# Performance work log

Hardware: AMD Instinct MI355X
Metric: run time of the kernel (lower is better)

The kernel has to match this reference:

```python
import jax, jax.numpy as jnp
import numpy as np


def _rot_mat(thetas, scales):
    # thetas, scales: [bs, g] -> [bs, g, 9, 9] bilinear-interpolation matrices
    bs, g = thetas.shape
    t = thetas.reshape(-1)
    s = scales.reshape(-1)
    x = jnp.cos(t) * s
    y = jnp.sin(t) * s
    yp = -y
    z = jnp.zeros_like(x)
    o = jnp.ones_like(x)
    a = x - y; b = x * y; c = x + y; d = a * c; e = a + c
    ap = x - yp; bp = x * yp; cp = x + yp; dp = ap * cp; ep = ap + cp

    def M(rows):
        # rows: 9 lists of 9 [N]-arrays -> [9, 9, N]
        return jnp.stack([jnp.stack(r, axis=0) for r in rows], axis=0)

    ctr = [z, z, z, z, o, z, z, z, z]

    pb1 = M([
        [a, 1 - a, z, z, z, z, z, z, z],
        [z, 1 - y, y, z, z, z, z, z, z],
        [z, z, a, z, z, 1 - a, z, z, z],
        [y, z, z, 1 - y, z, z, z, z, z],
        ctr,
        [z, z, z, z, z, 1 - y, z, z, y],
        [z, z, z, 1 - a, z, z, a, z, z],
        [z, z, z, z, z, z, y, 1 - y, z],
        [z, z, z, z, z, z, z, 1 - a, a]])
    pb2 = M([
        [a, 1 - a, z, z, z, z, z, z, z],
        [z, x - b, b, z, 1 - c + b, y - b, z, z, z],
        [z, z, a, z, z, 1 - a, z, z, z],
        [b, y - b, z, x - b, 1 - c + b, z, z, z, z],
        ctr,
        [z, z, z, z, 1 - c + b, x - b, z, y - b, b],
        [z, z, z, 1 - a, z, z, a, z, z],
        [z, z, z, y - b, 1 - c + b, z, b, x - b, z],
        [z, z, z, z, z, z, z, 1 - a, a]])
    ps1 = M([
        [d, a - d, z, c - d, 1 - e + d, z, z, z, z],
        [z, x - b, b, z, 1 - c + b, y - b, z, z, z],
        [z, c - d, d, z, 1 - e + d, a - d, z, z, z],
        [b, y - b, z, x - b, 1 - c + b, z, z, z, z],
        ctr,
        [z, z, z, z, 1 - c + b, x - b, z, y - b, b],
        [z, z, z, a - d, 1 - e + d, z, d, c - d, z],
        [z, z, z, y - b, 1 - c + b, z, b, x - b, z],
        [z, z, z, z, 1 - e + d, c - d, z, a - d, d]])
    ps2 = pb2  # identical in the source
    nb1 = M([
        [cp, z, z, 1 - cp, z, z, z, z, z],
        [yp, 1 - yp, z, z, z, z, z, z, z],
        [z, 1 - cp, cp, z, z, z, z, z, z],
        [z, z, z, 1 - yp, z, z, yp, z, z],
        ctr,
        [z, z, yp, z, z, 1 - yp, z, z, z],
        [z, z, z, z, z, z, cp, 1 - cp, z],
        [z, z, z, z, z, z, z, 1 - yp, yp],
        [z, z, z, z, z, 1 - cp, z, z, cp]])
    nb2 = M([
        [cp, z, z, 1 - cp, z, z, z, z, z],
        [bp, x - bp, z, yp - bp, 1 - cp + bp, z, z, z, z],
        [z, 1 - cp, cp, z, z, z, z, z, z],
        [z, z, z, x - bp, 1 - cp + bp, z, bp, yp - bp, z],
        ctr,
        [z, yp - bp, bp, z, 1 - cp + bp, x - bp, z, z, z],
        [z, z, z, z, z, z, cp, 1 - cp, z],
        [z, z, z, z, 1 - cp + bp, yp - bp, z, x - bp, bp],
        [z, z, z, z, z, 1 - cp, z, z, cp]])
    ns1 = M([
        [dp, cp - dp, z, ap - dp, 1 - ep + dp, z, z, z, z],
        [bp, x - bp, z, yp - bp, 1 - cp + bp, z, z, z, z],
        [z, ap - dp, dp, z, 1 - ep + dp, cp - dp, z, z, z],
        [z, yp - bp, bp, z, 1 - cp + bp, x - bp, z, z, z],
        ctr,
        [z, z, z, x - bp, 1 - cp + bp, z, bp, yp - bp, z],
        [z, z, z, cp - dp, 1 - ep + dp, z, dp, ap - dp, z],
        [z, z, z, z, 1 - cp + bp, yp - bp, z, x - bp, bp],
        [z, z, z, z, 1 - ep + dp, ap - dp, z, cp - dp, dp]])
    ns2 = nb2  # mirrors the positive branch where small_2 == big_2

    m_pos = (t >= 0.0)[None, None, :]
    m_big = (s >= 1.0)[None, None, :]
    m_1 = (jnp.abs(t) <= jnp.pi / 4)[None, None, :]
    pos = jnp.where(m_big, jnp.where(m_1, pb1, pb2), jnp.where(m_1, ps1, ps2))
    neg = jnp.where(m_big, jnp.where(m_1, nb1, nb2), jnp.where(m_1, ns1, ns2))
    rot = jnp.where(m_pos, pos, neg)  # [9, 9, bs*g]
    return jnp.transpose(rot, (2, 0, 1)).reshape(bs, g, 9, 9)


def _forward(x, thetas, scales, lambdas, weight):
    # x: [B, Cin, H, W]; weight: [n, Cout, Cin, 3, 3]; thetas/scales/lambdas: [B, n]
    B, Cin, H, W = x.shape
    n, Cout = weight.shape[0], weight.shape[1]
    rot = _rot_mat(thetas, scales) * lambdas[:, :, None, None]  # [B, n, 9, 9]
    w9 = weight.reshape(n, Cout, Cin, 9)
    # per-sample transformed kernel: sum over kernel_number n and source taps j
    w = jnp.einsum('bnij,nocj->bioc', rot, w9)  # [B, 9, Cout, Cin]
    w = jnp.transpose(w, (0, 2, 3, 1)).reshape(B * Cout, Cin, 3, 3)
    xg = x.reshape(1, B * Cin, H, W)
    out = jax.lax.conv_general_dilated(
        xg, w, window_strides=(1, 1), padding=((1, 1), (1, 1)),
        dimension_numbers=('NCHW', 'OIHW', 'NCHW'), feature_group_count=B)
    return out.reshape(B, Cout, H, W)


def setup_inputs() -> dict:
    key = jax.random.key(0)
    ks = jax.random.split(key, 5)
    B, Cin, Cout, H, W, n = 16, 256, 256, 64, 64, 4
    x = jax.random.normal(ks[0], (B, Cin, H, W), dtype=jnp.float32)
    thetas = jax.random.uniform(ks[1], (B, n), minval=-1.2, maxval=1.2, dtype=jnp.float32)
    scales = jax.random.uniform(ks[2], (B, n), minval=0.5, maxval=1.5, dtype=jnp.float32)
    lambdas = jax.nn.softmax(jax.random.normal(ks[3], (B, n), dtype=jnp.float32), axis=-1)
    weight = jax.random.normal(ks[4], (n, Cout, Cin, 3, 3), dtype=jnp.float32) * 0.05
    return {"x": x, "thetas": thetas, "scales": scales, "lambdas": lambdas, "weight": weight}


def reference(x, thetas, scales, lambdas, weight):
    return _forward(x, thetas, scales, lambdas, weight)
```

## Files before the change

### kernel.cpp

```cpp
#include <hip/hip_runtime.h>
#include <cstdint>
#include <cstddef>

typedef unsigned short ushort_t;
typedef __attribute__((ext_vector_type(4))) float f32x4;
typedef __attribute__((ext_vector_type(8))) short s16x8;

#define PI_4F 0.78539816339744830962f

__device__ inline ushort_t f2bf(float f) {
  unsigned int u = __float_as_uint(f);
  u = u + 0x7fffu + ((u >> 16) & 1u);
  return (ushort_t)(u >> 16);
}

__device__ void rot_compute(float t, float s, float* M) {
  float xv = cosf(t) * s, yv = sinf(t) * s;
  bool pos = (t >= 0.0f), big = (s >= 1.0f), m1 = (fabsf(t) <= PI_4F);
#pragma unroll
  for (int i = 0; i < 81; ++i) M[i] = 0.0f;
  M[36 + 4] = 1.0f;
  if (pos) {
    float a = xv - yv, bb = xv * yv, c = xv + yv;
    if (m1 && big) {
      M[0] = a; M[1] = 1 - a;
      M[9 + 1] = 1 - yv; M[9 + 2] = yv;
      M[18 + 2] = a; M[18 + 5] = 1 - a;
      M[27 + 0] = yv; M[27 + 3] = 1 - yv;
      M[45 + 5] = 1 - yv; M[45 + 8] = yv;
      M[54 + 3] = 1 - a; M[54 + 6] = a;
      M[63 + 6] = yv; M[63 + 7] = 1 - yv;
      M[72 + 7] = 1 - a; M[72 + 8] = a;
    } else if (m1) {
      float d = a * c, e = a + c;
      M[0] = d; M[1] = a - d; M[3] = c - d; M[4] = 1 - e + d;
      M[9 + 1] = xv - bb; M[9 + 2] = bb; M[9 + 4] = 1 - c + bb; M[9 + 5] = yv - bb;
      M[18 + 1] = c - d; M[18 + 2] = d; M[18 + 4] = 1 - e + d; M[18 + 5] = a - d;
      M[27 + 0] = bb; M[27 + 1] = yv - bb; M[27 + 3] = xv - bb; M[27 + 4] = 1 - c + bb;
      M[45 + 4] = 1 - c + bb; M[45 + 5] = xv - bb; M[45 + 7] = yv - bb; M[45 + 8] = bb;
      M[54 + 3] = a - d; M[54 + 4] = 1 - e + d; M[54 + 6] = d; M[54 + 7] = c - d;
      M[63 + 3] = yv - bb; M[63 + 4] = 1 - c + bb; M[63 + 6] = bb; M[63 + 7] = xv - bb;
      M[72 + 4] = 1 - e + d; M[72 + 5] = c - d; M[72 + 7] = a - d; M[72 + 8] = d;
    } else {
      M[0] = a; M[1] = 1 - a;
      M[9 + 1] = xv - bb; M[9 + 2] = bb; M[9 + 4] = 1 - c + bb; M[9 + 5] = yv - bb;
      M[18 + 2] = a; M[18 + 5] = 1 - a;
      M[27 + 0] = bb; M[27 + 1] = yv - bb; M[27 + 3] = xv - bb; M[27 + 4] = 1 - c + bb;
      M[45 + 4] = 1 - c + bb; M[45 + 5] = xv - bb; M[45 + 7] = yv - bb; M[45 + 8] = bb;
      M[54 + 3] = 1 - a; M[54 + 6] = a;
      M[63 + 3] = yv - bb; M[63 + 4] = 1 - c + bb; M[63 + 6] = bb; M[63 + 7] = xv - bb;
      M[72 + 7] = 1 - a; M[72 + 8] = a;
    }
  } else {
    float yp = -yv;
    float ap = xv - yp, bp = xv * yp, cp = xv + yp;
    if (m1 && big) {
      M[0] = cp; M[3] = 1 - cp;
      M[9 + 0] = yp; M[9 + 1] = 1 - yp;
      M[18 + 1] = 1 - cp; M[18 + 2] = cp;
      M[27 + 3] = 1 - yp; M[27 + 6] = yp;
      M[45 + 2] = yp; M[45 + 5] = 1 - yp;
      M[54 + 6] = cp; M[54 + 7] = 1 - cp;
      M[63 + 7] = 1 - yp; M[63 + 8] = yp;
      M[72 + 5] = 1 - cp; M[72 + 8] = cp;
    } else if (m1) {
      float dp = ap * cp, ep = ap + cp;
      M[0] = dp; M[1] = cp - dp; M[3] = ap - dp; M[4] = 1 - ep + dp;
      M[9 + 0] = bp; M[9 + 1] = xv - bp; M[9 + 3] = yp - bp; M[9 + 4] = 1 - cp + bp;
      M[18 + 1] = ap - dp; M[18 + 2] = dp; M[18 + 4] = 1 - ep + dp; M[18 + 5] = cp - dp;
      M[27 + 1] = yp - bp; M[27 + 2] = bp; M[27 + 4] = 1 - cp + bp; M[27 + 5] = xv - bp;
      M[45 + 3] = xv - bp; M[45 + 4] = 1 - cp + bp; M[45 + 6] = bp; M[45 + 7] = yp - bp;
      M[54 + 3] = cp - dp; M[54 + 4] = 1 - ep + dp; M[54 + 6] = dp; M[54 + 7] = ap - dp;
      M[63 + 4] = 1 - cp + bp; M[63 + 5] = yp - bp; M[63 + 7] = xv - bp; M[63 + 8] = bp;
      M[72 + 4] = 1 - ep + dp; M[72 + 5] = ap - dp; M[72 + 7] = cp - dp; M[72 + 8] = dp;
    } else {
      M[0] = cp; M[3] = 1 - cp;
      M[9 + 0] = bp; M[9 + 1] = xv - bp; M[9 + 3] = yp - bp; M[9 + 4] = 1 - cp + bp;
      M[18 + 1] = 1 - cp; M[18 + 2] = cp;
      M[27 + 3] = xv - bp; M[27 + 4] = 1 - cp + bp; M[27 + 6] = bp; M[27 + 7] = yp - bp;
      M[45 + 1] = yp - bp; M[45 + 2] = bp; M[45 + 4] = 1 - cp + bp; M[45 + 5] = xv - bp;
      M[54 + 6] = cp; M[54 + 7] = 1 - cp;
      M[63 + 4] = 1 - cp + bp; M[63 + 5] = yp - bp; M[63 + 7] = xv - bp; M[63 + 8] = bp;
      M[72 + 5] = 1 - cp; M[72 + 8] = cp;
    }
  }
}

__global__ __launch_bounds__(128) void wt_kernel(const float* __restrict__ weight,
                                                 const float* __restrict__ thetas,
                                                 const float* __restrict__ scales,
                                                 const float* __restrict__ lambdas,
                                                 ushort_t* __restrict__ wtout) {
  __shared__ float rotl[16][81];
  const int o = blockIdx.x, bg = blockIdx.y;
  const int tloc = threadIdx.x;
  const int c = tloc * 2;
  float wv0[4][9], wv1[4][9];
#pragma unroll
  for (int n = 0; n < 4; ++n) {
    const float* wp = weight + (((size_t)(n * 256 + o)) * 256 + c) * 9;
#pragma unroll
    for (int j = 0; j < 9; ++j) { wv0[n][j] = wp[j]; wv1[n][j] = wp[9 + j]; }
  }
  if (tloc < 16) {
    int gid = bg * 16 + tloc;
    float M[81];
    rot_compute(thetas[gid], scales[gid], M);
    float lam = lambdas[gid];
#pragma unroll
    for (int i = 0; i < 81; ++i) rotl[tloc][i] = M[i] * lam;
  }
  __syncthreads();
#pragma unroll
  for (int bl = 0; bl < 4; ++bl) {
    const int b = bg * 4 + bl;
#pragma unroll
    for (int i = 0; i < 9; ++i) {
      float a0 = 0.0f, a1 = 0.0f;
#pragma unroll
      for (int n = 0; n < 4; ++n) {
        const float* r = &rotl[bl * 4 + n][i * 9];
#pragma unroll
        for (int j = 0; j < 9; ++j) {
          a0 = fmaf(r[j], wv0[n][j], a0);
          a1 = fmaf(r[j], wv1[n][j], a1);
        }
      }
      unsigned int word = (unsigned int)f2bf(a0) | ((unsigned int)f2bf(a1) << 16);
      *(unsigned int*)&wtout[((size_t)((b * 9 + i) * 256 + o)) * 256 + c] = word;
    }
  }
}

__global__ __launch_bounds__(256) void transpose_kernel(const float* __restrict__ x,
                                                        ushort_t* __restrict__ xpad) {
  __shared__ ushort_t tile[64][68];
  const int b = blockIdx.z, ct = blockIdx.y, st = blockIdx.x;
  const int t = threadIdx.x;
  const int c0 = ct * 64;
  const float* xb = x + ((size_t)(b * 256 + c0)) * 4096 + st * 64;
#pragma unroll
  for (int k = 0; k < 4; ++k) {
    int idx = t + 256 * k;
    int c_l = idx >> 4, w4 = (idx & 15) * 4;
    float4 v = *(const float4*)&xb[(size_t)c_l * 4096 + w4];
    tile[w4 + 0][c_l] = f2bf(v.x);
    tile[w4 + 1][c_l] = f2bf(v.y);
    tile[w4 + 2][c_l] = f2bf(v.z);
    tile[w4 + 3][c_l] = f2bf(v.w);
  }
  __syncthreads();
  const int c4 = (t & 15) * 4, wl = t >> 4;
  const size_t rowbase = (size_t)(b * 4356 + (st + 1) * 66) * 256 + c0;
#pragma unroll
  for (int k = 0; k < 4; ++k) {
    int w = wl + 16 * k;
    uint2 v = *(const uint2*)&tile[w][c4];
    *(uint2*)&xpad[rowbase + (size_t)(w + 1) * 256 + c4] = v;
  }
  if (t < 32) {
    int w = (t & 16) ? 65 : 0;
    int cc = (t & 15) * 4;
    *(uint2*)&xpad[rowbase + (size_t)w * 256 + cc] = make_uint2(0u, 0u);
  }
  if (st == 0 || st == 63) {
    const int h = (st == 0) ? 0 : 65;
    const size_t hb = (size_t)(b * 4356 + h * 66) * 256 + c0;
    for (int idx = t; idx < 66 * 16; idx += 256) {
      int w = idx >> 4, cc = (idx & 15) * 4;
      *(uint2*)&xpad[hb + (size_t)w * 256 + cc] = make_uint2(0u, 0u);
    }
  }
}

__device__ inline void gload16(const ushort_t* g, ushort_t* l) {
  __builtin_amdgcn_global_load_lds(
      (const __attribute__((address_space(1))) unsigned int*)g,
      (__attribute__((address_space(3))) unsigned int*)l, 16, 0, 0);
}

#define WAITB(N)                                                      \
  asm volatile("s_waitcnt vmcnt(" #N ") lgkmcnt(0)\n\ts_barrier" ::: "memory")

__global__ __launch_bounds__(256, 2) void conv_kernel(
    const ushort_t* __restrict__ xpad, const ushort_t* __restrict__ wt,
    float* __restrict__ out) {
  __shared__ __align__(16) ushort_t As0[8192], As1[8192], As2[8192];
  __shared__ __align__(16) ushort_t Bs0[4096], Bs1[4096], Bs2[4096];

  const int id = blockIdx.x;
  const int xcd = id & 7;
  const int jj = id >> 3;
  const int b = xcd * 2 + (jj >> 5);
  const int ntile = jj & 31;

  const int t = threadIdx.x;
  const int wave = t >> 6, lane = t & 63;
  const int wm = wave & 1, wn = wave >> 1;
  const int lr = lane & 15, lq = lane >> 4;
  const int h0 = ntile * 2;

  const ushort_t* wt_b = wt + (size_t)b * 589824;
  const ushort_t* xp_b = xpad + (size_t)b * 1115136;

  const int lrow = t >> 2;
  const int cg8 = (((t & 3) ^ ((t >> 3) & 3)) * 8);
  const int rsw = (lr >> 1) & 3;
  const int aoff = (wm * 128 + lr) * 32 + ((lq ^ rsw) * 8);
  const int boff = (wn * 64 + lr) * 32 + ((lq ^ rsw) * 8);

  f32x4 acc[8][4];
#pragma unroll
  for (int i = 0; i < 8; ++i)
#pragma unroll
    for (int j2 = 0; j2 < 4; ++j2) acc[i][j2] = (f32x4)(0.0f);

  auto stage = [&](int ks, ushort_t* Ad, ushort_t* Bd) {
    const int tap = ks >> 3;
    const int c0k = (ks & 7) << 5;
    const int kh = tap / 3, kw = tap - kh * 3;
    const ushort_t* ga = wt_b + ((size_t)(tap * 256 + lrow)) * 256 + c0k + cg8;
    gload16(ga, Ad + wave * 512);
    gload16(ga + 64 * 256, Ad + 2048 + wave * 512);
    gload16(ga + 128 * 256, Ad + 4096 + wave * 512);
    gload16(ga + 192 * 256, Ad + 6144 + wave * 512);
    const int sp = (h0 + kh) * 66 + kw + lrow;
    gload16(xp_b + (size_t)sp * 256 + c0k + cg8, Bd + wave * 512);
    gload16(xp_b + (size_t)(sp + 66) * 256 + c0k + cg8, Bd + 2048 + wave * 512);
  };

  auto compute = [&](const ushort_t* Ab, const ushort_t* Bb) {
    s16x8 bfr[4];
#pragma unroll
    for (int ni = 0; ni < 4; ++ni)
      bfr[ni] = *(const s16x8*)(Bb + boff + ni * 512);
#pragma unroll
    for (int mi = 0; mi < 8; ++mi) {
      s16x8 af = *(const s16x8*)(Ab + aoff + mi * 512);
#pragma unroll
      for (int ni = 0; ni < 4; ++ni)
        acc[mi][ni] = __builtin_amdgcn_mfma_f32_16x16x32_bf16(af, bfr[ni], acc[mi][ni], 0, 0, 0);
    }
  };

  stage(0, As0, Bs0);
  stage(1, As1, Bs1);

#pragma unroll 1
  for (int kk = 0; kk < 23; ++kk) {
    const int ks = kk * 3;
    WAITB(6);
    stage(ks + 2, As2, Bs2);
    compute(As0, Bs0);
    WAITB(6);
    stage(ks + 3, As0, Bs0);
    compute(As1, Bs1);
    WAITB(6);
    stage(ks + 4, As1, Bs1);
    compute(As2, Bs2);
  }
  WAITB(6);
  stage(71, As2, Bs2);
  compute(As0, Bs0);
  WAITB(6);
  compute(As1, Bs1);
  WAITB(0);
  compute(As2, Bs2);

  float* ob = out + ((size_t)(b * 256 + wm * 128)) * 4096 + ntile * 128 + wn * 64 + lr;
#pragma unroll
  for (int mi = 0; mi < 8; ++mi)
#pragma unroll
    for (int r = 0; r < 4; ++r) {
      float* orow = ob + (size_t)(mi * 16 + lq * 4 + r) * 4096;
#pragma unroll
      for (int ni = 0; ni < 4; ++ni) orow[ni * 16] = acc[mi][ni][r];
    }
}

extern "C" void kernel_launch(void* const* d_in, const int* in_sizes, int n_in,
                              void* d_out, int out_size, void* d_ws, size_t ws_size,
                              hipStream_t stream) {
  const float* x = (const float*)d_in[0];
  const float* thetas = (const float*)d_in[1];
  const float* scales = (const float*)d_in[2];
  const float* lambdas = (const float*)d_in[3];
  const float* weight = (const float*)d_in[4];
  float* out = (float*)d_out;

  ushort_t* wt_ws = (ushort_t*)d_ws;
  ushort_t* xpad_ws = (ushort_t*)((char*)d_ws + 18874368);

  wt_kernel<<<dim3(256, 4), 128, 0, stream>>>(weight, thetas, scales, lambdas, wt_ws);
  transpose_kernel<<<dim3(64, 4, 16), 256, 0, stream>>>(x, xpad_ws);
  conv_kernel<<<512, 256, 0, stream>>>(xpad_ws, wt_ws, out);
}
```

Baseline: 215.8 us.

## Merge prep kernels into one launch and double-buffer MFMA fragments in conv loop

The weight-rotation kernel and the input transpose/pad kernel become one launch, with the block index selecting which job a block does. This removes a kernel launch and lets the two independent prep jobs run side by side. The conv main loop now software-pipelines its LDS fragment loads into two register sets, so the next stage's fragments are read while the current MFMAs run. This costs extra VGPRs (24 more fragment registers), which may hurt the two-waves-per-SIMD occupancy target, and the tail clamps the stage index to 71, issuing redundant loads.

Result: faster. 211.1 us (-2.2%).

```diff
diff --git a/kernel.cpp b/kernel.cpp
--- a/kernel.cpp
+++ b/kernel.cpp
@@ -86,89 +86,93 @@
   }
 }
 
-__global__ __launch_bounds__(128) void wt_kernel(const float* __restrict__ weight,
-                                                 const float* __restrict__ thetas,
-                                                 const float* __restrict__ scales,
-                                                 const float* __restrict__ lambdas,
-                                                 ushort_t* __restrict__ wtout) {
-  __shared__ float rotl[16][81];
-  const int o = blockIdx.x, bg = blockIdx.y;
-  const int tloc = threadIdx.x;
-  const int c = tloc * 2;
-  float wv0[4][9], wv1[4][9];
-#pragma unroll
-  for (int n = 0; n < 4; ++n) {
-    const float* wp = weight + (((size_t)(n * 256 + o)) * 256 + c) * 9;
-#pragma unroll
-    for (int j = 0; j < 9; ++j) { wv0[n][j] = wp[j]; wv1[n][j] = wp[9 + j]; }
-  }
-  if (tloc < 16) {
-    int gid = bg * 16 + tloc;
-    float M[81];
-    rot_compute(thetas[gid], scales[gid], M);
-    float lam = lambdas[gid];
-#pragma unroll
-    for (int i = 0; i < 81; ++i) rotl[tloc][i] = M[i] * lam;
-  }
-  __syncthreads();
-#pragma unroll
-  for (int bl = 0; bl < 4; ++bl) {
-    const int b = bg * 4 + bl;
-#pragma unroll
-    for (int i = 0; i < 9; ++i) {
-      float a0 = 0.0f, a1 = 0.0f;
-#pragma unroll
-      for (int n = 0; n < 4; ++n) {
-        const float* r = &rotl[bl * 4 + n][i * 9];
-#pragma unroll
-        for (int j = 0; j < 9; ++j) {
-          a0 = fmaf(r[j], wv0[n][j], a0);
-          a1 = fmaf(r[j], wv1[n][j], a1);
+__global__ __launch_bounds__(256) void prep_kernel(
+    const float* __restrict__ x, const float* __restrict__ weight,
+    const float* __restrict__ thetas, const float* __restrict__ scales,
+    const float* __restrict__ lambdas, ushort_t* __restrict__ xpad,
+    ushort_t* __restrict__ wtout) {
+  __shared__ __align__(16) char smem[64 * 68 * 2];
+  const int bi = blockIdx.x;
+  const int t = threadIdx.x;
+
+  if (bi < 512) {
+    float* rotl = (float*)smem;
+    const int bg = bi >> 7, o2 = bi & 127;
+    const int half = t >> 7, tloc = t & 127;
+    const int o = o2 * 2 + half;
+    const int c = tloc * 2;
+    float wv0[4][9], wv1[4][9];
+#pragma unroll
+    for (int n = 0; n < 4; ++n) {
+      const float* wp = weight + (((size_t)(n * 256 + o)) * 256 + c) * 9;
+#pragma unroll
+      for (int j = 0; j < 9; ++j) { wv0[n][j] = wp[j]; wv1[n][j] = wp[9 + j]; }
+    }
+    if (t < 16) {
+      int gid = bg * 16 + t;
+      float M[81];
+      rot_compute(thetas[gid], scales[gid], M);
+      float lam = lambdas[gid];
+#pragma unroll
+      for (int i = 0; i < 81; ++i) rotl[t * 81 + i] = M[i] * lam;
+    }
+    __syncthreads();
+#pragma unroll
+    for (int bl = 0; bl < 4; ++bl) {
+      const int b = bg * 4 + bl;
+#pragma unroll
+      for (int i = 0; i < 9; ++i) {
+        float a0 = 0.0f, a1 = 0.0f;
+#pragma unroll
+        for (int n = 0; n < 4; ++n) {
+          const float* r = &rotl[(bl * 4 + n) * 81 + i * 9];
+#pragma unroll
+          for (int j = 0; j < 9; ++j) {
+            a0 = fmaf(r[j], wv0[n][j], a0);
+            a1 = fmaf(r[j], wv1[n][j], a1);
+          }
         }
+        unsigned int word = (unsigned int)f2bf(a0) | ((unsigned int)f2bf(a1) << 16);
+        *(unsigned int*)&wtout[((size_t)((b * 9 + i) * 256 + o)) * 256 + c] = word;
       }
-      unsigned int word = (unsigned int)f2bf(a0) | ((unsigned int)f2bf(a1) << 16);
-      *(unsigned int*)&wtout[((size_t)((b * 9 + i) * 256 + o)) * 256 + c] = word;
-    }
-  }
-}
-
-__global__ __launch_bounds__(256) void transpose_kernel(const float* __restrict__ x,
-                                                        ushort_t* __restrict__ xpad) {
-  __shared__ ushort_t tile[64][68];
-  const int b = blockIdx.z, ct = blockIdx.y, st = blockIdx.x;
-  const int t = threadIdx.x;
-  const int c0 = ct * 64;
-  const float* xb = x + ((size_t)(b * 256 + c0)) * 4096 + st * 64;
-#pragma unroll
-  for (int k = 0; k < 4; ++k) {
-    int idx = t + 256 * k;
-    int c_l = idx >> 4, w4 = (idx & 15) * 4;
-    float4 v = *(const float4*)&xb[(size_t)c_l * 4096 + w4];
-    tile[w4 + 0][c_l] = f2bf(v.x);
-    tile[w4 + 1][c_l] = f2bf(v.y);
-    tile[w4 + 2][c_l] = f2bf(v.z);
-    tile[w4 + 3][c_l] = f2bf(v.w);
-  }
-  __syncthreads();
-  const int c4 = (t & 15) * 4, wl = t >> 4;
-  const size_t rowbase = (size_t)(b * 4356 + (st + 1) * 66) * 256 + c0;
-#pragma unroll
-  for (int k = 0; k < 4; ++k) {
-    int w = wl + 16 * k;
-    uint2 v = *(const uint2*)&tile[w][c4];
-    *(uint2*)&xpad[rowbase + (size_t)(w + 1) * 256 + c4] = v;
-  }
-  if (t < 32) {
-    int w = (t & 16) ? 65 : 0;
-    int cc = (t & 15) * 4;
-    *(uint2*)&xpad[rowbase + (size_t)w * 256 + cc] = make_uint2(0u, 0u);
-  }
-  if (st == 0 || st == 63) {
-    const int h = (st == 0) ? 0 : 65;
-    const size_t hb = (size_t)(b * 4356 + h * 66) * 256 + c0;
-    for (int idx = t; idx < 66 * 16; idx += 256) {
-      int w = idx >> 4, cc = (idx & 15) * 4;
-      *(uint2*)&xpad[hb + (size_t)w * 256 + cc] = make_uint2(0u, 0u);
+    }
+  } else {
+    ushort_t (*tile)[68] = (ushort_t(*)[68])smem;
+    const int bi2 = bi - 512;
+    const int b = bi2 >> 8, ct = (bi2 >> 6) & 3, st = bi2 & 63;
+    const int c0 = ct * 64;
+    const float* xb = x + ((size_t)(b * 256 + c0)) * 4096 + st * 64;
+#pragma unroll
+    for (int k = 0; k < 4; ++k) {
+      int idx = t + 256 * k;
+      int c_l = idx >> 4, w4 = (idx & 15) * 4;
+      float4 v = *(const float4*)&xb[(size_t)c_l * 4096 + w4];
+      tile[w4 + 0][c_l] = f2bf(v.x);
+      tile[w4 + 1][c_l] = f2bf(v.y);
+      tile[w4 + 2][c_l] = f2bf(v.z);
+      tile[w4 + 3][c_l] = f2bf(v.w);
+    }
+    __syncthreads();
+    const int c4 = (t & 15) * 4, wl = t >> 4;
+    const size_t rowbase = (size_t)(b * 4356 + (st + 1) * 66) * 256 + c0;
+#pragma unroll
+    for (int k = 0; k < 4; ++k) {
+      int w = wl + 16 * k;
+      uint2 v = *(const uint2*)&tile[w][c4];
+      *(uint2*)&xpad[rowbase + (size_t)(w + 1) * 256 + c4] = v;
+    }
+    if (t < 32) {
+      int w = (t & 16) ? 65 : 0;
+      int cc = (t & 15) * 4;
+      *(uint2*)&xpad[rowbase + (size_t)w * 256 + cc] = make_uint2(0u, 0u);
+    }
+    if (st == 0 || st == 63) {
+      const int h = (st == 0) ? 0 : 65;
+      const size_t hb = (size_t)(b * 4356 + h * 66) * 256 + c0;
+      for (int idx = t; idx < 66 * 16; idx += 256) {
+        int w = idx >> 4, cc = (idx & 15) * 4;
+        *(uint2*)&xpad[hb + (size_t)w * 256 + cc] = make_uint2(0u, 0u);
+      }
     }
   }
 }
@@ -214,6 +218,8 @@
   for (int i = 0; i < 8; ++i)
 #pragma unroll
     for (int j2 = 0; j2 < 4; ++j2) acc[i][j2] = (f32x4)(0.0f);
+
+  s16x8 af0[8], bf0[4], af1[8], bf1[4];
 
   auto stage = [&](int ks, ushort_t* Ad, ushort_t* Bd) {
     const int tap = ks >> 3;
@@ -229,43 +235,47 @@
     gload16(xp_b + (size_t)(sp + 66) * 256 + c0k + cg8, Bd + 2048 + wave * 512);
   };
 
-  auto compute = [&](const ushort_t* Ab, const ushort_t* Bb) {
-    s16x8 bfr[4];
-#pragma unroll
-    for (int ni = 0; ni < 4; ++ni)
-      bfr[ni] = *(const s16x8*)(Bb + boff + ni * 512);
-#pragma unroll
-    for (int mi = 0; mi < 8; ++mi) {
-      s16x8 af = *(const s16x8*)(Ab + aoff + mi * 512);
+  auto fragload = [&](const ushort_t* Ab, const ushort_t* Bb, s16x8* af, s16x8* bf) {
+#pragma unroll
+    for (int ni = 0; ni < 4; ++ni) bf[ni] = *(const s16x8*)(Bb + boff + ni * 512);
+#pragma unroll
+    for (int mi = 0; mi < 8; ++mi) af[mi] = *(const s16x8*)(Ab + aoff + mi * 512);
+  };
+
+  auto mfma_step = [&](const s16x8* af, const s16x8* bf) {
+#pragma unroll
+    for (int mi = 0; mi < 8; ++mi)
 #pragma unroll
       for (int ni = 0; ni < 4; ++ni)
-        acc[mi][ni] = __builtin_amdgcn_mfma_f32_16x16x32_bf16(af, bfr[ni], acc[mi][ni], 0, 0, 0);
-    }
+        acc[mi][ni] = __builtin_amdgcn_mfma_f32_16x16x32_bf16(af[mi], bf[ni], acc[mi][ni], 0, 0, 0);
   };
+
+#define STEP(KSS, SS, NS, AFC, BFC, AFN, BFN)                 \
+  WAITB(6);                                                   \
+  {                                                           \
+    const int kss_ = (KSS) > 71 ? 71 : (KSS);                 \
+    stage(kss_, As##SS, Bs##SS);                              \
+  }                                                           \
+  fragload(As##NS, Bs##NS, AFN, BFN);                         \
+  mfma_step(AFC, BFC);
 
   stage(0, As0, Bs0);
   stage(1, As1, Bs1);
+  stage(2, As2, Bs2);
+  asm volatile("s_waitcnt vmcnt(6) lgkmcnt(0)\n\ts_barrier" ::: "memory");
+  fragload(As0, Bs0, af0, bf0);
 
 #pragma unroll 1
-  for (int kk = 0; kk < 23; ++kk) {
-    const int ks = kk * 3;
-    WAITB(6);
-    stage(ks + 2, As2, Bs2);
-    compute(As0, Bs0);
-    WAITB(6);
-    stage(ks + 3, As0, Bs0);
-    compute(As1, Bs1);
-    WAITB(6);
-    stage(ks + 4, As1, Bs1);
-    compute(As2, Bs2);
+  for (int kk = 0; kk < 12; ++kk) {
+    const int ks0 = kk * 6;
+    STEP(ks0 + 3, 0, 1, af0, bf0, af1, bf1);
+    STEP(ks0 + 4, 1, 2, af1, bf1, af0, bf0);
+    STEP(ks0 + 5, 2, 0, af0, bf0, af1, bf1);
+    STEP(ks0 + 6, 0, 1, af1, bf1, af0, bf0);
+    STEP(ks0 + 7, 1, 2, af0, bf0, af1, bf1);
+    STEP(ks0 + 8, 2, 0, af1, bf1, af0, bf0);
   }
-  WAITB(6);
-  stage(71, As2, Bs2);
-  compute(As0, Bs0);
-  WAITB(6);
-  compute(As1, Bs1);
-  WAITB(0);
-  compute(As2, Bs2);
+#undef STEP
 
   float* ob = out + ((size_t)(b * 256 + wm * 128)) * 4096 + ntile * 128 + wn * 64 + lr;
 #pragma unroll
@@ -291,7 +301,7 @@
   ushort_t* wt_ws = (ushort_t*)d_ws;
   ushort_t* xpad_ws = (ushort_t*)((char*)d_ws + 18874368);
 
-  wt_kernel<<<dim3(256, 4), 128, 0, stream>>>(weight, thetas, scales, lambdas, wt_ws);
-  transpose_kernel<<<dim3(64, 4, 16), 256, 0, stream>>>(x, xpad_ws);
+  prep_kernel<<<4608, 256, 0, stream>>>(x, weight, thetas, scales, lambdas,
+                                        xpad_ws, wt_ws);
   conv_kernel<<<512, 256, 0, stream>>>(xpad_ws, wt_ws, out);
 }
```
